# Performance work log

Measured on AMD Instinct MI355X. Metric: run time of the kernel, lower is better.

The kernel has to match this reference:

```python
import jax, jax.numpy as jnp
import numpy as np

D_K = 64

def setup_inputs() -> dict:
    key = jax.random.key(0)
    kq, kk, kv = jax.random.split(key, 3)
    B, Lq, Lk, d = 32, 2048, 2048, D_K
    return {
        "query": jax.random.normal(kq, (B, Lq, d), dtype=jnp.float32),
        "key": jax.random.normal(kk, (B, Lk, d), dtype=jnp.float32),
        "value": jax.random.normal(kv, (B, Lk, d), dtype=jnp.float32),
    }

def reference(query, key, value):
    d_k = query.shape[-1]
    scale = 1.0 / jnp.sqrt(jnp.asarray(d_k, query.dtype))
    scores = jnp.einsum('nqd,nkd->nqk', query, key) * scale  # (B, Lq, Lk)
    attn = jax.nn.softmax(scores, axis=-1)  # masked=None -> plain softmax; dropout p=0.0 is identity
    return jnp.einsum('nqk,nkd->nqd', attn, value)  # (B, Lq, d_v)
```

## Files before the change

kernel.cpp:

```cpp
#include <hip/hip_runtime.h>


#define NB   32
#define LSEQ 2048
#define DH   64
#define BM   64
#define BN   64
#define NIT  (LSEQ / BN)

typedef __attribute__((ext_vector_type(8)))  __bf16 bf16x8;
typedef __attribute__((ext_vector_type(16))) float  f32x16;
typedef __attribute__((ext_vector_type(4)))  float  f32x4;
typedef __attribute__((ext_vector_type(2)))  unsigned uint2v;

union BF8 { bf16x8 v; unsigned short u[8]; unsigned u32[4]; uint4 q; };

__device__ __forceinline__ unsigned short f2bf(float f) {
    unsigned int u = __builtin_bit_cast(unsigned int, f);
    u += 0x7fffu + ((u >> 16) & 1u);
    return (unsigned short)(u >> 16);
}

__device__ __forceinline__ unsigned cvt_pk_bf16(float a, float b) {
    union { __bf16 h[2]; unsigned u; } t;
    t.h[0] = (__bf16)a; t.h[1] = (__bf16)b;
    return t.u;
}

__device__ __forceinline__ float fast_exp2(float x) {
#if __has_builtin(__builtin_amdgcn_exp2f)
    return __builtin_amdgcn_exp2f(x);
#else
    return exp2f(x);
#endif
}

#define KBLK ((NB * LSEQ * 8) / 256)
__global__ __launch_bounds__(256)
void prep(const float* __restrict__ Kg, const float* __restrict__ Vg,
          unsigned short* __restrict__ Kb, unsigned short* __restrict__ Vt) {
    __shared__ __align__(16) unsigned T2[64 * 36];
    const int tid = threadIdx.x;
    if (blockIdx.x < KBLK) {
        const int CH  = blockIdx.x * 256 + tid;
        const int b   = CH >> 14;
        const int rem = CH & 16383;
        const int n   = rem >> 3;
        const int cc  = rem & 7;
        const int c   = cc ^ (n & 7);
        const float* src = Kg + (((size_t)b * LSEQ + n) * DH + c * 8);
        float4 f0 = ((const float4*)src)[0];
        float4 f1 = ((const float4*)src)[1];
        BF8 t;
        t.u[0]=f2bf(f0.x); t.u[1]=f2bf(f0.y); t.u[2]=f2bf(f0.z); t.u[3]=f2bf(f0.w);
        t.u[4]=f2bf(f1.x); t.u[5]=f2bf(f1.y); t.u[6]=f2bf(f1.z); t.u[7]=f2bf(f1.w);
        *(bf16x8*)&Kb[(size_t)CH * 8] = t.v;
    } else {
        const int bx = blockIdx.x - KBLK;
        const int b  = bx >> 5;
        const int nt = bx & 31;
        const int n  = (tid >> 3) * 2;
        const int dc = (tid & 7) * 8;
        const float* s0 = Vg + (((size_t)b * LSEQ + nt * 64 + n) * DH + dc);
        float4 a0 = ((const float4*)s0)[0];
        float4 a1 = ((const float4*)s0)[1];
        const float* s1 = s0 + DH;
        float4 b0 = ((const float4*)s1)[0];
        float4 b1 = ((const float4*)s1)[1];
        float va[8] = {a0.x,a0.y,a0.z,a0.w, a1.x,a1.y,a1.z,a1.w};
        float vb[8] = {b0.x,b0.y,b0.z,b0.w, b1.x,b1.y,b1.z,b1.w};
        const int n2 = n >> 1;
        #pragma unroll
        for (int j = 0; j < 8; ++j)
            T2[(dc + j) * 36 + n2] = (unsigned)f2bf(va[j]) | ((unsigned)f2bf(vb[j]) << 16);
        __syncthreads();
        #pragma unroll
        for (int i = 0; i < 2; ++i) {
            const int CH = i * 256 + tid;
            const int cc = CH >> 6;
            const int d  = CH & 63;
            uint4 o = *(const uint4*)&T2[d * 36 + cc * 4];
            *(uint4*)&Vt[((((size_t)(b * 32 + nt)) * 8 + cc) * 64 + d) * 8] = o;
        }
    }
}

__global__ __launch_bounds__(256, 4)
void attn_fwd(const unsigned short* __restrict__ Kb,
              const unsigned short* __restrict__ Vt,
              const float* __restrict__ Qg,
              float* __restrict__ Og) {
    __shared__ __align__(16) char smem[18944];
    float* Mrg = (float*)smem;
    float* Lsh = (float*)(smem + 18432);

    const int tid  = threadIdx.x;
    const int lane = tid & 63;
    const int wave = tid >> 6;
    const int m32  = lane & 31;
    const int h    = lane >> 5;
    const int qh   = wave >> 1;
    const int kvh  = wave & 1;

    const int L  = blockIdx.y * 32 + blockIdx.x;
    const int Lp = (L & 7) * 128 + (L >> 3);
    const int b  = Lp >> 5;
    const int qt = Lp & 31;

    const float qscale = 0.18033688011112042f;
    const int qrow = qt * BM + qh * 32 + m32;
    bf16x8 qf[4];
    {
        const float* qp = Qg + ((size_t)(b * LSEQ + qrow)) * DH;
        #pragma unroll
        for (int kt = 0; kt < 4; ++kt) {
            const float* p4 = qp + kt * 16 + h * 8;
            f32x4 f0 = __builtin_nontemporal_load((const f32x4*)p4);
            f32x4 f1 = __builtin_nontemporal_load(((const f32x4*)p4) + 1);
            BF8 t;
            t.u[0]=f2bf(f0.x*qscale); t.u[1]=f2bf(f0.y*qscale);
            t.u[2]=f2bf(f0.z*qscale); t.u[3]=f2bf(f0.w*qscale);
            t.u[4]=f2bf(f1.x*qscale); t.u[5]=f2bf(f1.y*qscale);
            t.u[6]=f2bf(f1.z*qscale); t.u[7]=f2bf(f1.w*qscale);
            qf[kt] = t.v;
        }
    }

    int koff[4];
    #pragma unroll
    for (int kt = 0; kt < 4; ++kt) {
        const int n  = kvh * 32 + m32;
        const int cc = kt * 2 + h;
        koff[kt] = (n * 8 + (cc ^ (n & 7))) * 16;
    }

    const int v00 = (((kvh * 4 + 0 + h) * 64) +  0 + m32) * 16;
    const int v01 = (((kvh * 4 + 2 + h) * 64) +  0 + m32) * 16;
    const int v10 = (((kvh * 4 + 0 + h) * 64) + 32 + m32) * 16;
    const int v11 = (((kvh * 4 + 2 + h) * 64) + 32 + m32) * 16;

    const char* kgb = (const char*)Kb + (size_t)b * (LSEQ * DH * 2);
    const char* vgb = (const char*)Vt + (size_t)b * (DH * LSEQ * 2);

    BF8 kf[4], vf[4];
    #pragma unroll
    for (int kt = 0; kt < 4; ++kt) kf[kt].q = *(const uint4*)(kgb + koff[kt]);
    vf[0].q = *(const uint4*)(vgb + v00);
    vf[1].q = *(const uint4*)(vgb + v01);
    vf[2].q = *(const uint4*)(vgb + v10);
    vf[3].q = *(const uint4*)(vgb + v11);

    f32x16 o0, o1;
    #pragma unroll
    for (int i = 0; i < 16; ++i) { o0[i] = 0.f; o1[i] = 0.f; }
    float l_run = 0.f;

    for (int nt = 0; nt < NIT; ++nt) {
        f32x16 s;
        #pragma unroll
        for (int i = 0; i < 16; ++i) s[i] = 0.f;
        __builtin_amdgcn_s_setprio(1);
        #pragma unroll
        for (int kt = 0; kt < 4; ++kt)
            s = __builtin_amdgcn_mfma_f32_32x32x16_bf16(kf[kt].v, qf[kt], s, 0, 0, 0);
        __builtin_amdgcn_s_setprio(0);

        if (nt + 1 < NIT) {
            const char* kp = kgb + (nt + 1) * 8192;
            #pragma unroll
            for (int kt = 0; kt < 4; ++kt) kf[kt].q = *(const uint4*)(kp + koff[kt]);
        }

        unsigned pk[8];
        #pragma unroll
        for (int g = 0; g < 4; ++g) {
            float e0 = fast_exp2(s[4*g]);
            float e1 = fast_exp2(s[4*g+1]);
            float e2 = fast_exp2(s[4*g+2]);
            float e3 = fast_exp2(s[4*g+3]);
            l_run += ((e0 + e1) + (e2 + e3));
            pk[2*g]   = cvt_pk_bf16(e0, e1);
            pk[2*g+1] = cvt_pk_bf16(e2, e3);
        }

        BF8 p0, p1;
        {
            uint2v r;
            r = __builtin_amdgcn_permlane32_swap(pk[0], pk[2], false, false);
            p0.u32[0] = r[0]; p0.u32[2] = r[1];
            r = __builtin_amdgcn_permlane32_swap(pk[1], pk[3], false, false);
            p0.u32[1] = r[0]; p0.u32[3] = r[1];
            r = __builtin_amdgcn_permlane32_swap(pk[4], pk[6], false, false);
            p1.u32[0] = r[0]; p1.u32[2] = r[1];
            r = __builtin_amdgcn_permlane32_swap(pk[5], pk[7], false, false);
            p1.u32[1] = r[0]; p1.u32[3] = r[1];
        }

        __builtin_amdgcn_s_setprio(1);
        o0 = __builtin_amdgcn_mfma_f32_32x32x16_bf16(vf[0].v, p0.v, o0, 0, 0, 0);
        o0 = __builtin_amdgcn_mfma_f32_32x32x16_bf16(vf[1].v, p1.v, o0, 0, 0, 0);
        o1 = __builtin_amdgcn_mfma_f32_32x32x16_bf16(vf[2].v, p0.v, o1, 0, 0, 0);
        o1 = __builtin_amdgcn_mfma_f32_32x32x16_bf16(vf[3].v, p1.v, o1, 0, 0, 0);
        __builtin_amdgcn_s_setprio(0);

        if (nt + 1 < NIT) {
            const char* vp = vgb + (nt + 1) * 8192;
            vf[0].q = *(const uint4*)(vp + v00);
            vf[1].q = *(const uint4*)(vp + v01);
            vf[2].q = *(const uint4*)(vp + v10);
            vf[3].q = *(const uint4*)(vp + v11);
        }
    }

    const float l2 = l_run + __shfl_xor(l_run, 32, 64);
    __syncthreads();
    if (kvh) {
        float* mp = Mrg + ((size_t)qh * 64 + lane) * 36;
        #pragma unroll
        for (int g = 0; g < 4; ++g) {
            *(float4*)(mp + 4*g)      = (float4){o0[4*g], o0[4*g+1], o0[4*g+2], o0[4*g+3]};
            *(float4*)(mp + 16 + 4*g) = (float4){o1[4*g], o1[4*g+1], o1[4*g+2], o1[4*g+3]};
        }
        if (h == 0) Lsh[qh * 32 + m32] = l2;
    }
    __syncthreads();
    if (!kvh) {
        const float* mp = Mrg + ((size_t)qh * 64 + lane) * 36;
        #pragma unroll
        for (int g = 0; g < 4; ++g) {
            float4 a = *(const float4*)(mp + 4*g);
            float4 c = *(const float4*)(mp + 16 + 4*g);
            o0[4*g] += a.x; o0[4*g+1] += a.y; o0[4*g+2] += a.z; o0[4*g+3] += a.w;
            o1[4*g] += c.x; o1[4*g+1] += c.y; o1[4*g+2] += c.z; o1[4*g+3] += c.w;
        }
        const float inv = 1.0f / (l2 + Lsh[qh * 32 + m32]);
        float* op = Og + ((size_t)(b * LSEQ + qrow)) * DH;
        #pragma unroll
        for (int t = 0; t < 2; ++t)
            #pragma unroll
            for (int g = 0; g < 4; ++g) {
                f32x4 v;
                v.x = (t ? o1[4*g+0] : o0[4*g+0]) * inv;
                v.y = (t ? o1[4*g+1] : o0[4*g+1]) * inv;
                v.z = (t ? o1[4*g+2] : o0[4*g+2]) * inv;
                v.w = (t ? o1[4*g+3] : o0[4*g+3]) * inv;
                __builtin_nontemporal_store(v, (f32x4*)(op + t * 32 + g * 8 + h * 4));
            }
    }
}

extern "C" void kernel_launch(void* const* d_in, const int* in_sizes, int n_in,
                              void* d_out, int out_size, void* d_ws, size_t ws_size,
                              hipStream_t stream) {
    const float* Q = (const float*)d_in[0];
    const float* K = (const float*)d_in[1];
    const float* V = (const float*)d_in[2];
    float* O = (float*)d_out;

    unsigned short* Kb = (unsigned short*)d_ws;
    unsigned short* Vt = (unsigned short*)d_ws + 4u * 1024u * 1024u;

    prep<<<dim3(KBLK + NB * (LSEQ / 64)), dim3(256), 0, stream>>>(K, V, Kb, Vt);
    attn_fwd<<<dim3(LSEQ / BM, NB), dim3(256), 0, stream>>>(Kb, Vt, Q, O);
}
```

Baseline: 142.6 us.

## Split KV four ways per block with 32-row query tiles and LDS reduction

Each block now handles 32 query rows, and its four waves each take a distinct 32-key slice of every 128-key step instead of a 2x2 query/KV split. This doubles the grid, so the per-wave key/value traffic per output row changes. The V loads move from a next-iteration prefetch to an in-iteration load. The K preprocessing drops its XOR swizzle, and the end of the kernel becomes a four-way LDS reduction with coalesced output stores. The risks are load latency in the V MFMA path, since it is no longer prefetched, and higher total K/V reads across the grid.

```diff
diff --git a/kernel.cpp b/kernel.cpp
--- a/kernel.cpp
+++ b/kernel.cpp
@@ -4,8 +4,8 @@
 #define NB   32
 #define LSEQ 2048
 #define DH   64
-#define BM   64
-#define BN   64
+#define BM   32
+#define BN   128
 #define NIT  (LSEQ / BN)
 
 typedef __attribute__((ext_vector_type(8)))  __bf16 bf16x8;
@@ -43,12 +43,7 @@
     const int tid = threadIdx.x;
     if (blockIdx.x < KBLK) {
         const int CH  = blockIdx.x * 256 + tid;
-        const int b   = CH >> 14;
-        const int rem = CH & 16383;
-        const int n   = rem >> 3;
-        const int cc  = rem & 7;
-        const int c   = cc ^ (n & 7);
-        const float* src = Kg + (((size_t)b * LSEQ + n) * DH + c * 8);
+        const float* src = Kg + (size_t)CH * 8;
         float4 f0 = ((const float4*)src)[0];
         float4 f1 = ((const float4*)src)[1];
         BF8 t;
@@ -85,30 +80,28 @@
     }
 }
 
+#define PLSTR 68
 __global__ __launch_bounds__(256, 4)
 void attn_fwd(const unsigned short* __restrict__ Kb,
               const unsigned short* __restrict__ Vt,
               const float* __restrict__ Qg,
               float* __restrict__ Og) {
-    __shared__ __align__(16) char smem[18944];
-    float* Mrg = (float*)smem;
-    float* Lsh = (float*)(smem + 18432);
+    __shared__ __align__(16) float Plds[4 * 32 * PLSTR + 4 * 32];
+    float* Lsh = Plds + 4 * 32 * PLSTR;
 
     const int tid  = threadIdx.x;
     const int lane = tid & 63;
-    const int wave = tid >> 6;
+    const int kvq  = tid >> 6;
     const int m32  = lane & 31;
     const int h    = lane >> 5;
-    const int qh   = wave >> 1;
-    const int kvh  = wave & 1;
-
-    const int L  = blockIdx.y * 32 + blockIdx.x;
-    const int Lp = (L & 7) * 128 + (L >> 3);
-    const int b  = Lp >> 5;
-    const int qt = Lp & 31;
+
+    const int L  = blockIdx.y * 64 + blockIdx.x;
+    const int Lp = (L & 7) * 256 + (L >> 3);
+    const int b  = Lp >> 6;
+    const int qt = Lp & 63;
 
     const float qscale = 0.18033688011112042f;
-    const int qrow = qt * BM + qh * 32 + m32;
+    const int qrow = qt * BM + m32;
     bf16x8 qf[4];
     {
         const float* qp = Qg + ((size_t)(b * LSEQ + qrow)) * DH;
@@ -126,49 +119,53 @@
         }
     }
 
+    const int n0 = kvq * 32 + m32;
     int koff[4];
     #pragma unroll
-    for (int kt = 0; kt < 4; ++kt) {
-        const int n  = kvh * 32 + m32;
-        const int cc = kt * 2 + h;
-        koff[kt] = (n * 8 + (cc ^ (n & 7))) * 16;
-    }
-
-    const int v00 = (((kvh * 4 + 0 + h) * 64) +  0 + m32) * 16;
-    const int v01 = (((kvh * 4 + 2 + h) * 64) +  0 + m32) * 16;
-    const int v10 = (((kvh * 4 + 0 + h) * 64) + 32 + m32) * 16;
-    const int v11 = (((kvh * 4 + 2 + h) * 64) + 32 + m32) * 16;
+    for (int kt = 0; kt < 4; ++kt)
+        koff[kt] = n0 * 128 + (kt * 2 + h) * 16;
+
+    int voff[2][2];
+    #pragma unroll
+    for (int dt = 0; dt < 2; ++dt)
+        #pragma unroll
+        for (int kt = 0; kt < 2; ++kt)
+            voff[dt][kt] = ((((kvq >> 1) * 8 + (kvq & 1) * 4 + kt * 2 + h) * 64)
+                            + dt * 32 + m32) * 16;
 
     const char* kgb = (const char*)Kb + (size_t)b * (LSEQ * DH * 2);
     const char* vgb = (const char*)Vt + (size_t)b * (DH * LSEQ * 2);
 
-    BF8 kf[4], vf[4];
+    BF8 kf[4];
     #pragma unroll
     for (int kt = 0; kt < 4; ++kt) kf[kt].q = *(const uint4*)(kgb + koff[kt]);
-    vf[0].q = *(const uint4*)(vgb + v00);
-    vf[1].q = *(const uint4*)(vgb + v01);
-    vf[2].q = *(const uint4*)(vgb + v10);
-    vf[3].q = *(const uint4*)(vgb + v11);
-
-    f32x16 o0, o1;
-    #pragma unroll
-    for (int i = 0; i < 16; ++i) { o0[i] = 0.f; o1[i] = 0.f; }
+
+    f32x16 o0, o1, fz;
+    #pragma unroll
+    for (int i = 0; i < 16; ++i) { o0[i] = 0.f; o1[i] = 0.f; fz[i] = 0.f; }
     float l_run = 0.f;
 
     for (int nt = 0; nt < NIT; ++nt) {
-        f32x16 s;
-        #pragma unroll
-        for (int i = 0; i < 16; ++i) s[i] = 0.f;
         __builtin_amdgcn_s_setprio(1);
-        #pragma unroll
-        for (int kt = 0; kt < 4; ++kt)
-            s = __builtin_amdgcn_mfma_f32_32x32x16_bf16(kf[kt].v, qf[kt], s, 0, 0, 0);
+        f32x16 s = __builtin_amdgcn_mfma_f32_32x32x16_bf16(kf[0].v, qf[0], fz, 0, 0, 0);
+        s = __builtin_amdgcn_mfma_f32_32x32x16_bf16(kf[1].v, qf[1], s, 0, 0, 0);
+        s = __builtin_amdgcn_mfma_f32_32x32x16_bf16(kf[2].v, qf[2], s, 0, 0, 0);
+        s = __builtin_amdgcn_mfma_f32_32x32x16_bf16(kf[3].v, qf[3], s, 0, 0, 0);
         __builtin_amdgcn_s_setprio(0);
 
         if (nt + 1 < NIT) {
-            const char* kp = kgb + (nt + 1) * 8192;
+            const char* kp = kgb + (nt + 1) * 16384;
             #pragma unroll
             for (int kt = 0; kt < 4; ++kt) kf[kt].q = *(const uint4*)(kp + koff[kt]);
+        }
+
+        BF8 vf00, vf01, vf10, vf11;
+        {
+            const char* vp = vgb + nt * 16384;
+            vf00.q = *(const uint4*)(vp + voff[0][0]);
+            vf01.q = *(const uint4*)(vp + voff[0][1]);
+            vf10.q = *(const uint4*)(vp + voff[1][0]);
+            vf11.q = *(const uint4*)(vp + voff[1][1]);
         }
 
         unsigned pk[8];
@@ -197,55 +194,42 @@
         }
 
         __builtin_amdgcn_s_setprio(1);
-        o0 = __builtin_amdgcn_mfma_f32_32x32x16_bf16(vf[0].v, p0.v, o0, 0, 0, 0);
-        o0 = __builtin_amdgcn_mfma_f32_32x32x16_bf16(vf[1].v, p1.v, o0, 0, 0, 0);
-        o1 = __builtin_amdgcn_mfma_f32_32x32x16_bf16(vf[2].v, p0.v, o1, 0, 0, 0);
-        o1 = __builtin_amdgcn_mfma_f32_32x32x16_bf16(vf[3].v, p1.v, o1, 0, 0, 0);
+        o0 = __builtin_amdgcn_mfma_f32_32x32x16_bf16(vf00.v, p0.v, o0, 0, 0, 0);
+        o0 = __builtin_amdgcn_mfma_f32_32x32x16_bf16(vf01.v, p1.v, o0, 0, 0, 0);
+        o1 = __builtin_amdgcn_mfma_f32_32x32x16_bf16(vf10.v, p0.v, o1, 0, 0, 0);
+        o1 = __builtin_amdgcn_mfma_f32_32x32x16_bf16(vf11.v, p1.v, o1, 0, 0, 0);
         __builtin_amdgcn_s_setprio(0);
-
-        if (nt + 1 < NIT) {
-            const char* vp = vgb + (nt + 1) * 8192;
-            vf[0].q = *(const uint4*)(vp + v00);
-            vf[1].q = *(const uint4*)(vp + v01);
-            vf[2].q = *(const uint4*)(vp + v10);
-            vf[3].q = *(const uint4*)(vp + v11);
-        }
     }
 
     const float l2 = l_run + __shfl_xor(l_run, 32, 64);
+    {
+        float* mp = &Plds[(kvq * 32 + m32) * PLSTR];
+        #pragma unroll
+        for (int g = 0; g < 4; ++g) {
+            *(float4*)(mp + 8*g + 4*h)      = (float4){o0[4*g], o0[4*g+1], o0[4*g+2], o0[4*g+3]};
+            *(float4*)(mp + 32 + 8*g + 4*h) = (float4){o1[4*g], o1[4*g+1], o1[4*g+2], o1[4*g+3]};
+        }
+        if (h == 0) Lsh[kvq * 32 + m32] = l2;
+    }
     __syncthreads();
-    if (kvh) {
-        float* mp = Mrg + ((size_t)qh * 64 + lane) * 36;
-        #pragma unroll
-        for (int g = 0; g < 4; ++g) {
-            *(float4*)(mp + 4*g)      = (float4){o0[4*g], o0[4*g+1], o0[4*g+2], o0[4*g+3]};
-            *(float4*)(mp + 16 + 4*g) = (float4){o1[4*g], o1[4*g+1], o1[4*g+2], o1[4*g+3]};
-        }
-        if (h == 0) Lsh[qh * 32 + m32] = l2;
-    }
-    __syncthreads();
-    if (!kvh) {
-        const float* mp = Mrg + ((size_t)qh * 64 + lane) * 36;
-        #pragma unroll
-        for (int g = 0; g < 4; ++g) {
-            float4 a = *(const float4*)(mp + 4*g);
-            float4 c = *(const float4*)(mp + 16 + 4*g);
-            o0[4*g] += a.x; o0[4*g+1] += a.y; o0[4*g+2] += a.z; o0[4*g+3] += a.w;
-            o1[4*g] += c.x; o1[4*g+1] += c.y; o1[4*g+2] += c.z; o1[4*g+3] += c.w;
-        }
-        const float inv = 1.0f / (l2 + Lsh[qh * 32 + m32]);
-        float* op = Og + ((size_t)(b * LSEQ + qrow)) * DH;
-        #pragma unroll
-        for (int t = 0; t < 2; ++t)
-            #pragma unroll
-            for (int g = 0; g < 4; ++g) {
-                f32x4 v;
-                v.x = (t ? o1[4*g+0] : o0[4*g+0]) * inv;
-                v.y = (t ? o1[4*g+1] : o0[4*g+1]) * inv;
-                v.z = (t ? o1[4*g+2] : o0[4*g+2]) * inv;
-                v.w = (t ? o1[4*g+3] : o0[4*g+3]) * inv;
-                __builtin_nontemporal_store(v, (f32x4*)(op + t * 32 + g * 8 + h * 4));
-            }
+    {
+        const int q  = tid >> 3;
+        const int dg = (tid & 7) * 8;
+        float4 sa = {0,0,0,0}, sb = {0,0,0,0};
+        #pragma unroll
+        for (int k = 0; k < 4; ++k) {
+            const float* mp = &Plds[(k * 32 + q) * PLSTR + dg];
+            float4 a = *(const float4*)(mp);
+            float4 c = *(const float4*)(mp + 4);
+            sa.x += a.x; sa.y += a.y; sa.z += a.z; sa.w += a.w;
+            sb.x += c.x; sb.y += c.y; sb.z += c.z; sb.w += c.w;
+        }
+        const float inv = 1.0f / (Lsh[q] + Lsh[32 + q] + Lsh[64 + q] + Lsh[96 + q]);
+        float* op = Og + (((size_t)(b * LSEQ + qt * BM + q)) * DH + dg);
+        f32x4 va = { sa.x * inv, sa.y * inv, sa.z * inv, sa.w * inv };
+        f32x4 vb = { sb.x * inv, sb.y * inv, sb.z * inv, sb.w * inv };
+        __builtin_nontemporal_store(va, (f32x4*)op);
+        __builtin_nontemporal_store(vb, (f32x4*)(op + 4));
     }
 }
 
```

New measurement: 173.9 us. 22.0% more time.
